# Optimization experiments

Hardware: AMD Instinct MI355X
Metric: run time of the kernel (lower is better)

The kernel has to match this reference:

```python
import jax, jax.numpy as jnp
import numpy as np

N_NODES = 50000
N_EDGES = 800000
D = 128          # input_dim == output_dim
H = 2 * D        # hidden size = 2*output_dim
EPS = 1e-5       # BatchNorm1d eps


def _mlp(x, W1, b1, g1, beta1, W2, b2):
    # Linear -> BatchNorm1d (training-mode batch stats) -> ReLU -> Linear
    y = x @ W1 + b1
    mu = jnp.mean(y, axis=0)
    var = jnp.mean(jnp.square(y - mu), axis=0)  # biased var, as used for normalization
    y = (y - mu) * jax.lax.rsqrt(var + EPS) * g1 + beta1
    y = jax.nn.relu(y)
    return y @ W2 + b2


def setup_inputs() -> dict:
    key = jax.random.key(0)
    ks = jax.random.split(key, 16)
    h = jax.random.normal(ks[0], (N_NODES, D), dtype=jnp.float32)
    e = jax.random.normal(ks[1], (N_EDGES, D), dtype=jnp.float32)
    src = jax.random.randint(ks[2], (N_EDGES,), 0, N_NODES, dtype=jnp.int32)
    dst = jax.random.randint(ks[3], (N_EDGES,), 0, N_NODES, dtype=jnp.int32)

    def lin(k, fan_in, fan_out):
        return jax.random.normal(k, (fan_in, fan_out), dtype=jnp.float32) * (1.0 / np.sqrt(fan_in))

    params = {
        # mlp_bond: in 2D -> H -> D
        'W1b': lin(ks[4], 2 * D, H), 'b1b': jnp.zeros((H,), jnp.float32),
        'g1b': jnp.ones((H,), jnp.float32), 'beta1b': jnp.zeros((H,), jnp.float32),
        'W2b': lin(ks[5], H, D), 'b2b': jnp.zeros((D,), jnp.float32),
        # mlp_atom: in 2D -> H -> D
        'W1a': lin(ks[6], 2 * D, H), 'b1a': jnp.zeros((H,), jnp.float32),
        'g1a': jnp.ones((H,), jnp.float32), 'beta1a': jnp.zeros((H,), jnp.float32),
        'W2a': lin(ks[7], H, D), 'b2a': jnp.zeros((D,), jnp.float32),
    }
    return {'h': h, 'e': e, 'src': src, 'dst': dst, **params}


def reference(h, e, src, dst,
              W1b, b1b, g1b, beta1b, W2b, b2b,
              W1a, b1a, g1a, beta1a, W2a, b2a):
    # --- bond update: gather u_add_v, concat with e, MLP ---
    sum_h_edge = h[src] + h[dst]                              # [E, D]
    e_new = _mlp(jnp.concatenate([sum_h_edge, e], axis=-1),
                 W1b, b1b, g1b, beta1b, W2b, b2b)             # [E, D]

    # --- atom update: scatter-sum of src node feats and NEW edge feats to dst ---
    sum_h = jax.ops.segment_sum(h[src], dst, num_segments=N_NODES)   # copy_u + sum
    sum_e = jax.ops.segment_sum(e_new, dst, num_segments=N_NODES)   # copy_e + sum
    h_new = _mlp(jnp.concatenate([sum_h, sum_e], axis=-1),
                 W1a, b1a, g1a, beta1a, W2a, b2a)             # [N, D]

    # out_batch_norm=False, out_activation=None, residual=False, dropout=None
    return h_new, e_new
```

## Files before the change

kernel.cpp:

```cpp
#include <hip/hip_runtime.h>
#include <stdint.h>

#define DD 128
#define HH 256
#define EPSBN 1e-5f

typedef __attribute__((ext_vector_type(4))) float f32x4;
typedef __attribute__((ext_vector_type(8))) short s16x8;
typedef __attribute__((ext_vector_type(4))) short s16x4;

__device__ __forceinline__ unsigned short f2bf(float f){
  union{float f; unsigned u;} v; v.f=f;
  unsigned u = v.u + 0x7fffu + ((v.u>>16)&1u);
  return (unsigned short)(u>>16);
}
__device__ __forceinline__ float bf2f(unsigned short s){
  union{unsigned u; float f;} v; v.u=((unsigned)s)<<16; return v.f;
}
__device__ __forceinline__ int swz(int row, int kb){ return row*512 + (kb ^ ((row&7)<<4)); }

__global__ void wt_kernel(const float* __restrict__ W1b, const float* __restrict__ W2b,
                          const float* __restrict__ W1a, const float* __restrict__ W2a,
                          unsigned short* __restrict__ WT1b, unsigned short* __restrict__ WT2b,
                          unsigned short* __restrict__ WT1a, unsigned short* __restrict__ WT2a){
  int idx = blockIdx.x*256 + threadIdx.x;
  if (idx < 65536){ int n=idx>>8, k=idx&255; WT1b[n*256+k]=f2bf(W1b[k*256+n]); }
  else if (idx < 98304){ int t=idx-65536; int n=t>>8, k=t&255; WT2b[n*256+k]=f2bf(W2b[k*128+n]); }
  else if (idx < 163840){ int t=idx-98304; int n=t>>8, k=t&255; WT1a[n*256+k]=f2bf(W1a[k*256+n]); }
  else if (idx < 196608){ int t=idx-163840; int n=t>>8, k=t&255; WT2a[n*256+k]=f2bf(W2a[k*128+n]); }
}

__global__ void h2bf_kernel(const float* __restrict__ h, unsigned short* __restrict__ hb, int n8){
  int i = blockIdx.x*256 + threadIdx.x;
  if (i < n8){
    f32x4 a = *(const f32x4*)(h + (size_t)i*8);
    f32x4 b = *(const f32x4*)(h + (size_t)i*8 + 4);
    s16x8 p;
    #pragma unroll
    for (int q=0;q<4;q++){ p[q]=(short)f2bf(a[q]); p[4+q]=(short)f2bf(b[q]); }
    *(s16x8*)(hb + (size_t)i*8) = p;
  }
}

__global__ void hist_kernel(const int* __restrict__ dst, int* __restrict__ counts, int E){
  int i = blockIdx.x*256 + threadIdx.x;
  if (i < E) atomicAdd(&counts[dst[i]], 1);
}

__global__ void scan_kernel(const int* __restrict__ counts, int* __restrict__ offsets,
                            int* __restrict__ cursor, int n){
  __shared__ int wsum[16];
  int tid = threadIdx.x, lane = tid&63, wid = tid>>6;
  int carry = 0;
  int nch = (n + 1023)/1024;
  for (int ch=0; ch<nch; ch++){
    int i = ch*1024 + tid;
    int v = (i<n)? counts[i] : 0;
    int s = v;
    #pragma unroll
    for (int off=1; off<64; off<<=1){ int t = __shfl_up(s, off); if (lane>=off) s += t; }
    if (lane==63) wsum[wid] = s;
    __syncthreads();
    int woff = 0, tot = 0;
    #pragma unroll
    for (int w=0; w<16; w++){ int t = wsum[w]; if (w<wid) woff += t; tot += t; }
    if (i<n){ int excl = carry + woff + s - v; offsets[i]=excl; cursor[i]=excl; }
    carry += tot;
    __syncthreads();
  }
  if (tid==0) offsets[n] = carry;
}

__global__ void fill_kernel(const int* __restrict__ dst, int* __restrict__ cursor,
                            int* __restrict__ eids, int E){
  int i = blockIdx.x*256 + threadIdx.x;
  if (i < E){ int slot = atomicAdd(&cursor[dst[i]], 1); eids[slot] = i; }
}

__device__ __forceinline__ void gemm1_core(char* xt, const s16x8 (&Bf)[8][2],
                                           float bias0, float bias1,
                                           unsigned short* __restrict__ yout,
                                           float* __restrict__ stats,
                                           int base, int nrows)
{
  const int tid = threadIdx.x;
  const int l = tid&63, w = tid>>6, lr = l&15, lg = l>>4;
  const int nb = w*32;
  f32x4 acc[4][2];
  #pragma unroll
  for (int mt=0;mt<4;mt++)
    #pragma unroll
    for (int nt=0;nt<2;nt++) acc[mt][nt] = (f32x4){0.f,0.f,0.f,0.f};
  #pragma unroll
  for (int kc=0;kc<8;kc++){
    s16x8 af[4];
    #pragma unroll
    for (int mt=0;mt<4;mt++)
      af[mt] = *(const s16x8*)(xt + swz(mt*16 + lr, kc*64 + lg*16));
    #pragma unroll
    for (int nt=0;nt<2;nt++)
      #pragma unroll
      for (int mt=0;mt<4;mt++)
        acc[mt][nt] = __builtin_amdgcn_mfma_f32_16x16x32_bf16(af[mt], Bf[kc][nt], acc[mt][nt], 0,0,0);
  }
  float st1a=0.f, st1b=0.f, st2a=0.f, st2b=0.f;
  #pragma unroll
  for (int mt=0;mt<4;mt++)
    #pragma unroll
    for (int q=0;q<4;q++){
      float m = (base + mt*16 + lg*4 + q < nrows) ? 1.0f : 0.0f;
      float v0 = (acc[mt][0][q] + bias0)*m;
      float v1 = (acc[mt][1][q] + bias1)*m;
      st1a += v0; st2a += v0*v0;
      st1b += v1; st2b += v1*v1;
    }
  __syncthreads();
  #pragma unroll
  for (int mt=0;mt<4;mt++)
    #pragma unroll
    for (int q=0;q<4;q++){
      *(unsigned short*)(xt + (mt*16 + lg*4 + q)*512 + (nb + lr)*2)      = f2bf(acc[mt][0][q] + bias0);
      *(unsigned short*)(xt + (mt*16 + lg*4 + q)*512 + (nb + 16 + lr)*2) = f2bf(acc[mt][1][q] + bias1);
    }
  __syncthreads();
  #pragma unroll
  for (int it=0;it<4;it++){
    int off = it*8192 + tid*16;
    int row = off >> 9;
    if (base + row < nrows)
      *(s16x8*)((char*)yout + (size_t)base*512 + off) = *(const s16x8*)(xt + off);
  }
  {
    int rep = blockIdx.x & 63;
    float s;
    s = st1a; s += __shfl_xor(s,16); s += __shfl_xor(s,32);
    if (l < 16) atomicAdd(&stats[rep*512 + nb + lr], s);
    s = st2a; s += __shfl_xor(s,16); s += __shfl_xor(s,32);
    if (l < 16) atomicAdd(&stats[rep*512 + 256 + nb + lr], s);
    s = st1b; s += __shfl_xor(s,16); s += __shfl_xor(s,32);
    if (l < 16) atomicAdd(&stats[rep*512 + nb + 16 + lr], s);
    s = st2b; s += __shfl_xor(s,16); s += __shfl_xor(s,32);
    if (l < 16) atomicAdd(&stats[rep*512 + 256 + nb + 16 + lr], s);
  }
}

__global__ __launch_bounds__(512, 4) void edge_mlp1(
    const unsigned short* __restrict__ hb, const float* __restrict__ e,
    const int* __restrict__ src, const int* __restrict__ dstv,
    const unsigned short* __restrict__ WT1, const float* __restrict__ b1,
    unsigned short* __restrict__ yout, float* __restrict__ stats, int E)
{
  __shared__ alignas(16) char xt[32768];
  const int tid = threadIdx.x;
  const int l = tid&63, w = tid>>6, lr = l&15, lg = l>>4;
  const int nb = w*32;
  const int base = blockIdx.x*64;

  {
    const int cb = tid&31, r0 = tid>>5;
    #pragma unroll
    for (int k=0;k<4;k++){
      int r = r0 + k*16;
      f32x4 v = *(const f32x4*)(e + (size_t)(base+r)*DD + cb*4);
      s16x4 p;
      #pragma unroll
      for (int q=0;q<4;q++) p[q] = (short)f2bf(v[q]);
      *(s16x4*)(xt + swz(r, 256 + cb*8)) = p;
    }
  }
  {
    const int r = tid>>3, jj = tid&7;
    const int ei = base + r;
    int s_ = src[ei], d_ = dstv[ei];
    const s16x8* hs = (const s16x8*)(hb + (size_t)s_*DD) + jj*2;
    const s16x8* hd = (const s16x8*)(hb + (size_t)d_*DD) + jj*2;
    s16x8 a0=hs[0], a1=hs[1], c0=hd[0], c1=hd[1];
    s16x8 o0, o1;
    #pragma unroll
    for (int q=0;q<8;q++){
      o0[q] = (short)f2bf(bf2f((unsigned short)a0[q]) + bf2f((unsigned short)c0[q]));
      o1[q] = (short)f2bf(bf2f((unsigned short)a1[q]) + bf2f((unsigned short)c1[q]));
    }
    *(s16x8*)(xt + swz(r, jj*32))      = o0;
    *(s16x8*)(xt + swz(r, jj*32 + 16)) = o1;
  }
  s16x8 Bf[8][2];
  #pragma unroll
  for (int kc=0;kc<8;kc++)
    #pragma unroll
    for (int nt=0;nt<2;nt++)
      Bf[kc][nt] = *(const s16x8*)(WT1 + (size_t)(nb + nt*16 + lr)*256 + kc*32 + lg*8);
  float bias0 = b1[nb+lr], bias1 = b1[nb+16+lr];
  __syncthreads();
  gemm1_core(xt, Bf, bias0, bias1, yout, stats, base, E);
}

__global__ __launch_bounds__(512, 2) void node_mlp1(
    const unsigned short* __restrict__ hb, const float* __restrict__ enew,
    const int* __restrict__ src, const int* __restrict__ offsets, const int* __restrict__ eids,
    const unsigned short* __restrict__ WT1, const float* __restrict__ b1,
    unsigned short* __restrict__ yout, float* __restrict__ stats, int NN)
{
  __shared__ alignas(16) char xt[32768];
  const int tid = threadIdx.x;
  const int l = tid&63, w = tid>>6, lr = l&15, lg = l>>4;
  const int nb = w*32;
  const int base = blockIdx.x*64;
  const int r = tid>>3, jj = tid&7;
  const int node = base + r;

  float ah[16], ae[16];
  #pragma unroll
  for (int q=0;q<16;q++){ ah[q]=0.f; ae[q]=0.f; }
  if (node < NN){
    int beg = offsets[node], end = offsets[node+1];
    for (int p=beg;p<end;p++){
      int eid = eids[p];
      int s_ = src[eid];
      const s16x8* hs = (const s16x8*)(hb + (size_t)s_*DD + jj*16);
      const f32x4* ep = (const f32x4*)(enew + (size_t)eid*DD + jj*16);
      s16x8 a0 = hs[0], a1 = hs[1];
      f32x4 e0 = ep[0], e1 = ep[1], e2 = ep[2], e3 = ep[3];
      #pragma unroll
      for (int q=0;q<8;q++){ ah[q] += bf2f((unsigned short)a0[q]); ah[8+q] += bf2f((unsigned short)a1[q]); }
      #pragma unroll
      for (int q=0;q<4;q++){ ae[q] += e0[q]; ae[4+q] += e1[q]; ae[8+q] += e2[q]; ae[12+q] += e3[q]; }
    }
  }
  {
    s16x8 o0, o1;
    #pragma unroll
    for (int q=0;q<8;q++){ o0[q] = (short)f2bf(ah[q]); o1[q] = (short)f2bf(ah[8+q]); }
    *(s16x8*)(xt + swz(r, jj*32))      = o0;
    *(s16x8*)(xt + swz(r, jj*32 + 16)) = o1;
    #pragma unroll
    for (int q=0;q<8;q++){ o0[q] = (short)f2bf(ae[q]); o1[q] = (short)f2bf(ae[8+q]); }
    *(s16x8*)(xt + swz(r, 256 + jj*32))      = o0;
    *(s16x8*)(xt + swz(r, 256 + jj*32 + 16)) = o1;
  }
  s16x8 Bf[8][2];
  #pragma unroll
  for (int kc=0;kc<8;kc++)
    #pragma unroll
    for (int nt=0;nt<2;nt++)
      Bf[kc][nt] = *(const s16x8*)(WT1 + (size_t)(nb + nt*16 + lr)*256 + kc*32 + lg*8);
  float bias0 = b1[nb+lr], bias1 = b1[nb+16+lr];
  __syncthreads();
  gemm1_core(xt, Bf, bias0, bias1, yout, stats, base, NN);
}

__global__ void finalize_kernel(const float* __restrict__ stats, const float* __restrict__ g,
                                const float* __restrict__ beta, float* __restrict__ scale, float invcnt){
  __shared__ float red[512];
  int tid = threadIdx.x;
  float s = 0.f;
  for (int rep=0; rep<64; rep++) s += stats[rep*512 + tid];
  red[tid] = s;
  __syncthreads();
  if (tid < 256){
    float mu  = red[tid]*invcnt;
    float var = red[256+tid]*invcnt - mu*mu;
    float a = g[tid] * rsqrtf(var + EPSBN);
    float c = beta[tid] - mu*a;
    scale[2*tid] = a; scale[2*tid+1] = c;
  }
}

__global__ __launch_bounds__(512, 4) void mlp2_kernel(const unsigned short* y,
    const unsigned short* __restrict__ WT2, const float* __restrict__ b2,
    const float* __restrict__ scale, float* outp, int nrows)
{
  __shared__ alignas(16) char xt[32768];
  const int tid = threadIdx.x;
  const int l = tid&63, w = tid>>6, lr = l&15, lg = l>>4;
  const int nb = w*16;
  const int base = blockIdx.x*64;

  const int cb = tid&31, r0 = tid>>5;
  float sa[8], sc[8];
  #pragma unroll
  for (int q=0;q<8;q++){ sa[q]=scale[2*(cb*8+q)]; sc[q]=scale[2*(cb*8+q)+1]; }
  #pragma unroll
  for (int k=0;k<4;k++){
    int r = r0 + k*16;
    s16x8 raw = {0,0,0,0,0,0,0,0};
    if (base + r < nrows) raw = *(const s16x8*)(y + (size_t)(base+r)*HH + cb*8);
    s16x8 o;
    #pragma unroll
    for (int q=0;q<8;q++){
      float f = fmaxf(bf2f((unsigned short)raw[q])*sa[q] + sc[q], 0.0f);
      o[q] = (short)f2bf(f);
    }
    *(s16x8*)(xt + swz(r, cb*16)) = o;
  }
  s16x8 Bf[8];
  #pragma unroll
  for (int kc=0;kc<8;kc++)
    Bf[kc] = *(const s16x8*)(WT2 + (size_t)(nb + lr)*HH + kc*32 + lg*8);
  float bias = b2[nb+lr];
  __syncthreads();

  f32x4 acc[4];
  #pragma unroll
  for (int mt=0;mt<4;mt++) acc[mt] = (f32x4){0.f,0.f,0.f,0.f};
  #pragma unroll
  for (int kc=0;kc<8;kc++){
    s16x8 af[4];
    #pragma unroll
    for (int mt=0;mt<4;mt++)
      af[mt] = *(const s16x8*)(xt + swz(mt*16 + lr, kc*64 + lg*16));
    #pragma unroll
    for (int mt=0;mt<4;mt++)
      acc[mt] = __builtin_amdgcn_mfma_f32_16x16x32_bf16(af[mt], Bf[kc], acc[mt], 0,0,0);
  }
  __syncthreads();
  #pragma unroll
  for (int mt=0;mt<4;mt++)
    #pragma unroll
    for (int q=0;q<4;q++)
      *(float*)(xt + (mt*16 + lg*4 + q)*512 + (nb + lr)*4) = acc[mt][q] + bias;
  __syncthreads();
  #pragma unroll
  for (int it=0;it<4;it++){
    int off = it*8192 + tid*16;
    int row = off >> 9;
    if (base + row < nrows)
      *(f32x4*)(outp + (size_t)(base+row)*DD + ((off&511)>>2)) = *(const f32x4*)(xt + off);
  }
}

extern "C" void kernel_launch(void* const* d_in, const int* in_sizes, int n_in,
                              void* d_out, int out_size, void* d_ws, size_t ws_size,
                              hipStream_t stream) {
  const float* h    = (const float*)d_in[0];
  const float* e    = (const float*)d_in[1];
  const int*   src  = (const int*)d_in[2];
  const int*   dst  = (const int*)d_in[3];
  const float* W1b  = (const float*)d_in[4];
  const float* b1b  = (const float*)d_in[5];
  const float* g1b  = (const float*)d_in[6];
  const float* beta1b=(const float*)d_in[7];
  const float* W2b  = (const float*)d_in[8];
  const float* b2b  = (const float*)d_in[9];
  const float* W1a  = (const float*)d_in[10];
  const float* b1a  = (const float*)d_in[11];
  const float* g1a  = (const float*)d_in[12];
  const float* beta1a=(const float*)d_in[13];
  const float* W2a  = (const float*)d_in[14];
  const float* b2a  = (const float*)d_in[15];

  const int E  = in_sizes[2];
  const int NN = in_sizes[0] / DD;

  char* ws = (char*)d_ws;
  unsigned short* WT1b = (unsigned short*)(ws + 0);
  unsigned short* WT2b = (unsigned short*)(ws + 131072);
  unsigned short* WT1a = (unsigned short*)(ws + 196608);
  unsigned short* WT2a = (unsigned short*)(ws + 327680);
  float* scaleE = (float*)(ws + 393216);
  float* scaleN = (float*)(ws + 395264);
  float* statsE = (float*)(ws + 397312);
  float* statsN = (float*)(ws + 528384);
  int* counts  = (int*)(ws + 659456);
  int* offsets = (int*)(ws + 860160);
  int* cursor  = (int*)(ws + 1060864);
  int* eids    = (int*)(ws + 1261568);
  unsigned short* ya = (unsigned short*)(ws + 4461568);
  unsigned short* hb = (unsigned short*)(ws + 30086144);

  float* outH = (float*)d_out;
  float* outE = outH + (size_t)NN * DD;
  unsigned short* yE = (unsigned short*)outE;

  hipMemsetAsync(ws + 397312, 0, 131072 + 131072 + 200704, stream);

  wt_kernel<<<768, 256, 0, stream>>>(W1b, W2b, W1a, W2a, WT1b, WT2b, WT1a, WT2a);
  h2bf_kernel<<<(NN*DD/8 + 255)/256, 256, 0, stream>>>(h, hb, NN*DD/8);
  hist_kernel<<<(E+255)/256, 256, 0, stream>>>(dst, counts, E);
  scan_kernel<<<1, 1024, 0, stream>>>(counts, offsets, cursor, NN);
  fill_kernel<<<(E+255)/256, 256, 0, stream>>>(dst, cursor, eids, E);

  const int tE = E/64;
  const int tN = (NN + 63)/64;

  edge_mlp1<<<tE, 512, 0, stream>>>(hb, e, src, dst, WT1b, b1b, yE, statsE, E);
  finalize_kernel<<<1, 512, 0, stream>>>(statsE, g1b, beta1b, scaleE, 1.0f/(float)E);
  mlp2_kernel<<<tE, 512, 0, stream>>>(yE, WT2b, b2b, scaleE, outE, E);
  node_mlp1<<<tN, 512, 0, stream>>>(hb, outE, src, offsets, eids, WT1a, b1a, ya, statsN, NN);
  finalize_kernel<<<1, 512, 0, stream>>>(statsN, g1a, beta1a, scaleN, 1.0f/(float)NN);
  mlp2_kernel<<<tN, 512, 0, stream>>>(ya, WT2a, b2a, scaleN, outH, NN);
}
```

Before: 800.5 us.

## Split node gather from GEMM, process two tiles per block, widen swizzle

The node MLP's first stage is split in two. A separate high-occupancy gather kernel accumulates the per-node h and e sums into a bf16 buffer, which reuses the output region as scratch, and a plain GEMM kernel then reads that buffer. Before, the gather ran inside a 2-waves-per-SIMD GEMM kernel. Edge MLP1 and MLP2 now process two 64-row tiles per block, so the weight fragments are loaded once per block and amortised over more rows. The swizzle XOR is widened from 3 to 5 row bits, and f2bf now calls the HIP intrinsic. These changes add an extra global round-trip for the node inputs, and the new swizzle could change LDS bank behaviour in either direction.

```diff
diff --git a/kernel.cpp b/kernel.cpp
--- a/kernel.cpp
+++ b/kernel.cpp
@@ -1,4 +1,5 @@
 #include <hip/hip_runtime.h>
+#include <hip/hip_bf16.h>
 #include <stdint.h>
 
 #define DD 128
@@ -10,14 +11,14 @@
 typedef __attribute__((ext_vector_type(4))) short s16x4;
 
 __device__ __forceinline__ unsigned short f2bf(float f){
-  union{float f; unsigned u;} v; v.f=f;
-  unsigned u = v.u + 0x7fffu + ((v.u>>16)&1u);
-  return (unsigned short)(u>>16);
+  union { __hip_bfloat16 h; unsigned short u; } v;
+  v.h = __float2bfloat16(f);
+  return v.u;
 }
 __device__ __forceinline__ float bf2f(unsigned short s){
   union{unsigned u; float f;} v; v.u=((unsigned)s)<<16; return v.f;
 }
-__device__ __forceinline__ int swz(int row, int kb){ return row*512 + (kb ^ ((row&7)<<4)); }
+__device__ __forceinline__ int swz(int row, int kb){ return row*512 + (kb ^ ((row&31)<<4)); }
 
 __global__ void wt_kernel(const float* __restrict__ W1b, const float* __restrict__ W2b,
                           const float* __restrict__ W1a, const float* __restrict__ W2a,
@@ -77,58 +78,109 @@
   if (i < E){ int slot = atomicAdd(&cursor[dst[i]], 1); eids[slot] = i; }
 }
 
-__device__ __forceinline__ void gemm1_core(char* xt, const s16x8 (&Bf)[8][2],
-                                           float bias0, float bias1,
-                                           unsigned short* __restrict__ yout,
-                                           float* __restrict__ stats,
-                                           int base, int nrows)
-{
+__device__ __forceinline__ void stage_edge_tile(char* xt,
+    const unsigned short* __restrict__ hb, const float* __restrict__ e,
+    const int* __restrict__ src, const int* __restrict__ dstv, int base)
+{
+  const int tid = threadIdx.x;
+  {
+    const int cb = tid&31, r0 = tid>>5;
+    #pragma unroll
+    for (int k=0;k<4;k++){
+      int r = r0 + k*16;
+      f32x4 v = *(const f32x4*)(e + (size_t)(base+r)*DD + cb*4);
+      s16x4 p;
+      #pragma unroll
+      for (int q=0;q<4;q++) p[q] = (short)f2bf(v[q]);
+      *(s16x4*)(xt + swz(r, 256 + cb*8)) = p;
+    }
+  }
+  {
+    const int r = tid>>3, jj = tid&7;
+    const int ei = base + r;
+    int s_ = src[ei], d_ = dstv[ei];
+    const s16x8* hs = (const s16x8*)(hb + (size_t)s_*DD) + jj*2;
+    const s16x8* hd = (const s16x8*)(hb + (size_t)d_*DD) + jj*2;
+    s16x8 a0=hs[0], a1=hs[1], c0=hd[0], c1=hd[1];
+    s16x8 o0, o1;
+    #pragma unroll
+    for (int q=0;q<8;q++){
+      o0[q] = (short)f2bf(bf2f((unsigned short)a0[q]) + bf2f((unsigned short)c0[q]));
+      o1[q] = (short)f2bf(bf2f((unsigned short)a1[q]) + bf2f((unsigned short)c1[q]));
+    }
+    *(s16x8*)(xt + swz(r, jj*32))      = o0;
+    *(s16x8*)(xt + swz(r, jj*32 + 16)) = o1;
+  }
+}
+
+__global__ __launch_bounds__(512, 4) void edge_mlp1(
+    const unsigned short* __restrict__ hb, const float* __restrict__ e,
+    const int* __restrict__ src, const int* __restrict__ dstv,
+    const unsigned short* __restrict__ WT1, const float* __restrict__ b1,
+    unsigned short* __restrict__ yout, float* __restrict__ stats, int E)
+{
+  __shared__ alignas(16) char xt[32768];
   const int tid = threadIdx.x;
   const int l = tid&63, w = tid>>6, lr = l&15, lg = l>>4;
   const int nb = w*32;
-  f32x4 acc[4][2];
-  #pragma unroll
-  for (int mt=0;mt<4;mt++)
-    #pragma unroll
-    for (int nt=0;nt<2;nt++) acc[mt][nt] = (f32x4){0.f,0.f,0.f,0.f};
-  #pragma unroll
-  for (int kc=0;kc<8;kc++){
-    s16x8 af[4];
+  const int base0 = blockIdx.x*128;
+
+  s16x8 Bf[8][2];
+  #pragma unroll
+  for (int kc=0;kc<8;kc++)
+    #pragma unroll
+    for (int nt=0;nt<2;nt++)
+      Bf[kc][nt] = *(const s16x8*)(WT1 + (size_t)(nb + nt*16 + lr)*256 + kc*32 + lg*8);
+  float bias0 = b1[nb+lr], bias1 = b1[nb+16+lr];
+
+  float st1a=0.f, st1b=0.f, st2a=0.f, st2b=0.f;
+
+  #pragma unroll 1
+  for (int t=0;t<2;t++){
+    const int base = base0 + t*64;
+    stage_edge_tile(xt, hb, e, src, dstv, base);
+    __syncthreads();
+    f32x4 acc[4][2];
     #pragma unroll
     for (int mt=0;mt<4;mt++)
-      af[mt] = *(const s16x8*)(xt + swz(mt*16 + lr, kc*64 + lg*16));
-    #pragma unroll
-    for (int nt=0;nt<2;nt++)
+      #pragma unroll
+      for (int nt=0;nt<2;nt++) acc[mt][nt] = (f32x4){0.f,0.f,0.f,0.f};
+    #pragma unroll
+    for (int kc=0;kc<8;kc++){
+      s16x8 af[4];
       #pragma unroll
       for (int mt=0;mt<4;mt++)
-        acc[mt][nt] = __builtin_amdgcn_mfma_f32_16x16x32_bf16(af[mt], Bf[kc][nt], acc[mt][nt], 0,0,0);
-  }
-  float st1a=0.f, st1b=0.f, st2a=0.f, st2b=0.f;
-  #pragma unroll
-  for (int mt=0;mt<4;mt++)
-    #pragma unroll
-    for (int q=0;q<4;q++){
-      float m = (base + mt*16 + lg*4 + q < nrows) ? 1.0f : 0.0f;
-      float v0 = (acc[mt][0][q] + bias0)*m;
-      float v1 = (acc[mt][1][q] + bias1)*m;
-      st1a += v0; st2a += v0*v0;
-      st1b += v1; st2b += v1*v1;
-    }
-  __syncthreads();
-  #pragma unroll
-  for (int mt=0;mt<4;mt++)
-    #pragma unroll
-    for (int q=0;q<4;q++){
-      *(unsigned short*)(xt + (mt*16 + lg*4 + q)*512 + (nb + lr)*2)      = f2bf(acc[mt][0][q] + bias0);
-      *(unsigned short*)(xt + (mt*16 + lg*4 + q)*512 + (nb + 16 + lr)*2) = f2bf(acc[mt][1][q] + bias1);
-    }
-  __syncthreads();
-  #pragma unroll
-  for (int it=0;it<4;it++){
-    int off = it*8192 + tid*16;
-    int row = off >> 9;
-    if (base + row < nrows)
+        af[mt] = *(const s16x8*)(xt + swz(mt*16 + lr, kc*64 + lg*16));
+      #pragma unroll
+      for (int nt=0;nt<2;nt++)
+        #pragma unroll
+        for (int mt=0;mt<4;mt++)
+          acc[mt][nt] = __builtin_amdgcn_mfma_f32_16x16x32_bf16(af[mt], Bf[kc][nt], acc[mt][nt], 0,0,0);
+    }
+    #pragma unroll
+    for (int mt=0;mt<4;mt++)
+      #pragma unroll
+      for (int q=0;q<4;q++){
+        float v0 = acc[mt][0][q] + bias0;
+        float v1 = acc[mt][1][q] + bias1;
+        st1a += v0; st2a += v0*v0;
+        st1b += v1; st2b += v1*v1;
+      }
+    __syncthreads();
+    #pragma unroll
+    for (int mt=0;mt<4;mt++)
+      #pragma unroll
+      for (int q=0;q<4;q++){
+        *(unsigned short*)(xt + (mt*16 + lg*4 + q)*512 + (nb + lr)*2)      = f2bf(acc[mt][0][q] + bias0);
+        *(unsigned short*)(xt + (mt*16 + lg*4 + q)*512 + (nb + 16 + lr)*2) = f2bf(acc[mt][1][q] + bias1);
+      }
+    __syncthreads();
+    #pragma unroll
+    for (int it=0;it<4;it++){
+      int off = it*8192 + tid*16;
       *(s16x8*)((char*)yout + (size_t)base*512 + off) = *(const s16x8*)(xt + off);
+    }
+    if (t==0) __syncthreads();
   }
   {
     int rep = blockIdx.x & 63;
@@ -144,11 +196,181 @@
   }
 }
 
-__global__ __launch_bounds__(512, 4) void edge_mlp1(
-    const unsigned short* __restrict__ hb, const float* __restrict__ e,
-    const int* __restrict__ src, const int* __restrict__ dstv,
+__global__ __launch_bounds__(512, 4) void mlp2_kernel(const unsigned short* y,
+    const unsigned short* __restrict__ WT2, const float* __restrict__ b2,
+    const float* __restrict__ scale, float* outp, int nrows)
+{
+  __shared__ alignas(16) char xt[32768];
+  const int tid = threadIdx.x;
+  const int l = tid&63, w = tid>>6, lr = l&15, lg = l>>4;
+  const int nb = w*16;
+  const int base0 = blockIdx.x*128;
+
+  s16x8 Bf[8];
+  #pragma unroll
+  for (int kc=0;kc<8;kc++)
+    Bf[kc] = *(const s16x8*)(WT2 + (size_t)(nb + lr)*HH + kc*32 + lg*8);
+  float bias = b2[nb+lr];
+  const int cb = tid&31, r0 = tid>>5;
+  float sa[8], sc[8];
+  #pragma unroll
+  for (int q=0;q<8;q++){ sa[q]=scale[2*(cb*8+q)]; sc[q]=scale[2*(cb*8+q)+1]; }
+
+  #pragma unroll 1
+  for (int t=0;t<2;t++){
+    const int base = base0 + t*64;
+    #pragma unroll
+    for (int k=0;k<4;k++){
+      int r = r0 + k*16;
+      s16x8 raw = {0,0,0,0,0,0,0,0};
+      if (base + r < nrows) raw = *(const s16x8*)(y + (size_t)(base+r)*HH + cb*8);
+      s16x8 o;
+      #pragma unroll
+      for (int q=0;q<8;q++){
+        float f = fmaxf(bf2f((unsigned short)raw[q])*sa[q] + sc[q], 0.0f);
+        o[q] = (short)f2bf(f);
+      }
+      *(s16x8*)(xt + swz(r, cb*16)) = o;
+    }
+    __syncthreads();
+    f32x4 acc[4];
+    #pragma unroll
+    for (int mt=0;mt<4;mt++) acc[mt] = (f32x4){0.f,0.f,0.f,0.f};
+    #pragma unroll
+    for (int kc=0;kc<8;kc++){
+      s16x8 af[4];
+      #pragma unroll
+      for (int mt=0;mt<4;mt++)
+        af[mt] = *(const s16x8*)(xt + swz(mt*16 + lr, kc*64 + lg*16));
+      #pragma unroll
+      for (int mt=0;mt<4;mt++)
+        acc[mt] = __builtin_amdgcn_mfma_f32_16x16x32_bf16(af[mt], Bf[kc], acc[mt], 0,0,0);
+    }
+    __syncthreads();
+    #pragma unroll
+    for (int mt=0;mt<4;mt++)
+      #pragma unroll
+      for (int q=0;q<4;q++)
+        *(float*)(xt + (mt*16 + lg*4 + q)*512 + (nb + lr)*4) = acc[mt][q] + bias;
+    __syncthreads();
+    #pragma unroll
+    for (int it=0;it<4;it++){
+      int off = it*8192 + tid*16;
+      int row = off >> 9;
+      if (base + row < nrows)
+        *(f32x4*)(outp + (size_t)(base+row)*DD + ((off&511)>>2)) = *(const f32x4*)(xt + off);
+    }
+    if (t==0) __syncthreads();
+  }
+}
+
+__global__ __launch_bounds__(256, 8) void node_gather(
+    const unsigned short* __restrict__ hb, const float* __restrict__ enew,
+    const int* __restrict__ src, const int* __restrict__ offsets, const int* __restrict__ eids,
+    unsigned short* __restrict__ xnode, int NN)
+{
+  const int tid = threadIdx.x;
+  const int r = tid>>3, jj = tid&7;
+  const int node = blockIdx.x*32 + r;
+  if (node >= NN) return;
+  float ah[16], ae[16];
+  #pragma unroll
+  for (int q=0;q<16;q++){ ah[q]=0.f; ae[q]=0.f; }
+  int beg = offsets[node], end = offsets[node+1];
+  for (int p=beg;p<end;p++){
+    int eid = eids[p];
+    int s_ = src[eid];
+    const s16x8* hs = (const s16x8*)(hb + (size_t)s_*DD + jj*16);
+    const f32x4* ep = (const f32x4*)(enew + (size_t)eid*DD + jj*16);
+    s16x8 a0 = hs[0], a1 = hs[1];
+    f32x4 e0 = ep[0], e1 = ep[1], e2 = ep[2], e3 = ep[3];
+    #pragma unroll
+    for (int q=0;q<8;q++){ ah[q] += bf2f((unsigned short)a0[q]); ah[8+q] += bf2f((unsigned short)a1[q]); }
+    #pragma unroll
+    for (int q=0;q<4;q++){ ae[q] += e0[q]; ae[4+q] += e1[q]; ae[8+q] += e2[q]; ae[12+q] += e3[q]; }
+  }
+  s16x8 o0, o1;
+  #pragma unroll
+  for (int q=0;q<8;q++){ o0[q] = (short)f2bf(ah[q]); o1[q] = (short)f2bf(ah[8+q]); }
+  *(s16x8*)(xnode + (size_t)node*HH + jj*16)     = o0;
+  *(s16x8*)(xnode + (size_t)node*HH + jj*16 + 8) = o1;
+  #pragma unroll
+  for (int q=0;q<8;q++){ o0[q] = (short)f2bf(ae[q]); o1[q] = (short)f2bf(ae[8+q]); }
+  *(s16x8*)(xnode + (size_t)node*HH + 128 + jj*16)     = o0;
+  *(s16x8*)(xnode + (size_t)node*HH + 128 + jj*16 + 8) = o1;
+}
+
+__device__ __forceinline__ void gemm1_core(char* xt, const s16x8 (&Bf)[8][2],
+                                           float bias0, float bias1,
+                                           unsigned short* __restrict__ yout,
+                                           float* __restrict__ stats,
+                                           int base, int nrows)
+{
+  const int tid = threadIdx.x;
+  const int l = tid&63, w = tid>>6, lr = l&15, lg = l>>4;
+  const int nb = w*32;
+  f32x4 acc[4][2];
+  #pragma unroll
+  for (int mt=0;mt<4;mt++)
+    #pragma unroll
+    for (int nt=0;nt<2;nt++) acc[mt][nt] = (f32x4){0.f,0.f,0.f,0.f};
+  #pragma unroll
+  for (int kc=0;kc<8;kc++){
+    s16x8 af[4];
+    #pragma unroll
+    for (int mt=0;mt<4;mt++)
+      af[mt] = *(const s16x8*)(xt + swz(mt*16 + lr, kc*64 + lg*16));
+    #pragma unroll
+    for (int nt=0;nt<2;nt++)
+      #pragma unroll
+      for (int mt=0;mt<4;mt++)
+        acc[mt][nt] = __builtin_amdgcn_mfma_f32_16x16x32_bf16(af[mt], Bf[kc][nt], acc[mt][nt], 0,0,0);
+  }
+  float st1a=0.f, st1b=0.f, st2a=0.f, st2b=0.f;
+  #pragma unroll
+  for (int mt=0;mt<4;mt++)
+    #pragma unroll
+    for (int q=0;q<4;q++){
+      float m = (base + mt*16 + lg*4 + q < nrows) ? 1.0f : 0.0f;
+      float v0 = (acc[mt][0][q] + bias0)*m;
+      float v1 = (acc[mt][1][q] + bias1)*m;
+      st1a += v0; st2a += v0*v0;
+      st1b += v1; st2b += v1*v1;
+    }
+  __syncthreads();
+  #pragma unroll
+  for (int mt=0;mt<4;mt++)
+    #pragma unroll
+    for (int q=0;q<4;q++){
+      *(unsigned short*)(xt + (mt*16 + lg*4 + q)*512 + (nb + lr)*2)      = f2bf(acc[mt][0][q] + bias0);
+      *(unsigned short*)(xt + (mt*16 + lg*4 + q)*512 + (nb + 16 + lr)*2) = f2bf(acc[mt][1][q] + bias1);
+    }
+  __syncthreads();
+  #pragma unroll
+  for (int it=0;it<4;it++){
+    int off = it*8192 + tid*16;
+    int row = off >> 9;
+    if (base + row < nrows)
+      *(s16x8*)((char*)yout + (size_t)base*512 + off) = *(const s16x8*)(xt + off);
+  }
+  {
+    int rep = blockIdx.x & 63;
+    float s;
+    s = st1a; s += __shfl_xor(s,16); s += __shfl_xor(s,32);
+    if (l < 16) atomicAdd(&stats[rep*512 + nb + lr], s);
+    s = st2a; s += __shfl_xor(s,16); s += __shfl_xor(s,32);
+    if (l < 16) atomicAdd(&stats[rep*512 + 256 + nb + lr], s);
+    s = st1b; s += __shfl_xor(s,16); s += __shfl_xor(s,32);
+    if (l < 16) atomicAdd(&stats[rep*512 + nb + 16 + lr], s);
+    s = st2b; s += __shfl_xor(s,16); s += __shfl_xor(s,32);
+    if (l < 16) atomicAdd(&stats[rep*512 + 256 + nb + 16 + lr], s);
+  }
+}
+
+__global__ __launch_bounds__(512, 4) void node_gemm1(
+    const unsigned short* __restrict__ xnode,
     const unsigned short* __restrict__ WT1, const float* __restrict__ b1,
-    unsigned short* __restrict__ yout, float* __restrict__ stats, int E)
+    unsigned short* __restrict__ yout, float* __restrict__ stats, int NN)
 {
   __shared__ alignas(16) char xt[32768];
   const int tid = threadIdx.x;
@@ -156,87 +378,13 @@
   const int nb = w*32;
   const int base = blockIdx.x*64;
 
-  {
-    const int cb = tid&31, r0 = tid>>5;
-    #pragma unroll
-    for (int k=0;k<4;k++){
-      int r = r0 + k*16;
-      f32x4 v = *(const f32x4*)(e + (size_t)(base+r)*DD + cb*4);
-      s16x4 p;
-      #pragma unroll
-      for (int q=0;q<4;q++) p[q] = (short)f2bf(v[q]);
-      *(s16x4*)(xt + swz(r, 256 + cb*8)) = p;
-    }
-  }
-  {
-    const int r = tid>>3, jj = tid&7;
-    const int ei = base + r;
-    int s_ = src[ei], d_ = dstv[ei];
-    const s16x8* hs = (const s16x8*)(hb + (size_t)s_*DD) + jj*2;
-    const s16x8* hd = (const s16x8*)(hb + (size_t)d_*DD) + jj*2;
-    s16x8 a0=hs[0], a1=hs[1], c0=hd[0], c1=hd[1];
-    s16x8 o0, o1;
-    #pragma unroll
-    for (int q=0;q<8;q++){
-      o0[q] = (short)f2bf(bf2f((unsigned short)a0[q]) + bf2f((unsigned short)c0[q]));
-      o1[q] = (short)f2bf(bf2f((unsigned short)a1[q]) + bf2f((unsigned short)c1[q]));
-    }
-    *(s16x8*)(xt + swz(r, jj*32))      = o0;
-    *(s16x8*)(xt + swz(r, jj*32 + 16)) = o1;
-  }
-  s16x8 Bf[8][2];
-  #pragma unroll
-  for (int kc=0;kc<8;kc++)
-    #pragma unroll
-    for (int nt=0;nt<2;nt++)
-      Bf[kc][nt] = *(const s16x8*)(WT1 + (size_t)(nb + nt*16 + lr)*256 + kc*32 + lg*8);
-  float bias0 = b1[nb+lr], bias1 = b1[nb+16+lr];
-  __syncthreads();
-  gemm1_core(xt, Bf, bias0, bias1, yout, stats, base, E);
-}
-
-__global__ __launch_bounds__(512, 2) void node_mlp1(
-    const unsigned short* __restrict__ hb, const float* __restrict__ enew,
-    const int* __restrict__ src, const int* __restrict__ offsets, const int* __restrict__ eids,
-    const unsigned short* __restrict__ WT1, const float* __restrict__ b1,
-    unsigned short* __restrict__ yout, float* __restrict__ stats, int NN)
-{
-  __shared__ alignas(16) char xt[32768];
-  const int tid = threadIdx.x;
-  const int l = tid&63, w = tid>>6, lr = l&15, lg = l>>4;
-  const int nb = w*32;
-  const int base = blockIdx.x*64;
-  const int r = tid>>3, jj = tid&7;
-  const int node = base + r;
-
-  float ah[16], ae[16];
-  #pragma unroll
-  for (int q=0;q<16;q++){ ah[q]=0.f; ae[q]=0.f; }
-  if (node < NN){
-    int beg = offsets[node], end = offsets[node+1];
-    for (int p=beg;p<end;p++){
-      int eid = eids[p];
-      int s_ = src[eid];
-      const s16x8* hs = (const s16x8*)(hb + (size_t)s_*DD + jj*16);
-      const f32x4* ep = (const f32x4*)(enew + (size_t)eid*DD + jj*16);
-      s16x8 a0 = hs[0], a1 = hs[1];
-      f32x4 e0 = ep[0], e1 = ep[1], e2 = ep[2], e3 = ep[3];
-      #pragma unroll
-      for (int q=0;q<8;q++){ ah[q] += bf2f((unsigned short)a0[q]); ah[8+q] += bf2f((unsigned short)a1[q]); }
-      #pragma unroll
-      for (int q=0;q<4;q++){ ae[q] += e0[q]; ae[4+q] += e1[q]; ae[8+q] += e2[q]; ae[12+q] += e3[q]; }
-    }
-  }
-  {
-    s16x8 o0, o1;
-    #pragma unroll
-    for (int q=0;q<8;q++){ o0[q] = (short)f2bf(ah[q]); o1[q] = (short)f2bf(ah[8+q]); }
-    *(s16x8*)(xt + swz(r, jj*32))      = o0;
-    *(s16x8*)(xt + swz(r, jj*32 + 16)) = o1;
-    #pragma unroll
-    for (int q=0;q<8;q++){ o0[q] = (short)f2bf(ae[q]); o1[q] = (short)f2bf(ae[8+q]); }
-    *(s16x8*)(xt + swz(r, 256 + jj*32))      = o0;
-    *(s16x8*)(xt + swz(r, 256 + jj*32 + 16)) = o1;
+  #pragma unroll
+  for (int it=0;it<4;it++){
+    int off = it*8192 + tid*16;
+    int row = off >> 9, kb = off & 511;
+    s16x8 v = {0,0,0,0,0,0,0,0};
+    if (base + row < NN) v = *(const s16x8*)((const char*)xnode + (size_t)base*512 + off);
+    *(s16x8*)(xt + swz(row, kb)) = v;
   }
   s16x8 Bf[8][2];
   #pragma unroll
@@ -263,69 +411,6 @@
     float a = g[tid] * rsqrtf(var + EPSBN);
     float c = beta[tid] - mu*a;
     scale[2*tid] = a; scale[2*tid+1] = c;
-  }
-}
-
-__global__ __launch_bounds__(512, 4) void mlp2_kernel(const unsigned short* y,
-    const unsigned short* __restrict__ WT2, const float* __restrict__ b2,
-    const float* __restrict__ scale, float* outp, int nrows)
-{
-  __shared__ alignas(16) char xt[32768];
-  const int tid = threadIdx.x;
-  const int l = tid&63, w = tid>>6, lr = l&15, lg = l>>4;
-  const int nb = w*16;
-  const int base = blockIdx.x*64;
-
-  const int cb = tid&31, r0 = tid>>5;
-  float sa[8], sc[8];
-  #pragma unroll
-  for (int q=0;q<8;q++){ sa[q]=scale[2*(cb*8+q)]; sc[q]=scale[2*(cb*8+q)+1]; }
-  #pragma unroll
-  for (int k=0;k<4;k++){
-    int r = r0 + k*16;
-    s16x8 raw = {0,0,0,0,0,0,0,0};
-    if (base + r < nrows) raw = *(const s16x8*)(y + (size_t)(base+r)*HH + cb*8);
-    s16x8 o;
-    #pragma unroll
-    for (int q=0;q<8;q++){
-      float f = fmaxf(bf2f((unsigned short)raw[q])*sa[q] + sc[q], 0.0f);
-      o[q] = (short)f2bf(f);
-    }
-    *(s16x8*)(xt + swz(r, cb*16)) = o;
-  }
-  s16x8 Bf[8];
-  #pragma unroll
-  for (int kc=0;kc<8;kc++)
-    Bf[kc] = *(const s16x8*)(WT2 + (size_t)(nb + lr)*HH + kc*32 + lg*8);
-  float bias = b2[nb+lr];
-  __syncthreads();
-
-  f32x4 acc[4];
-  #pragma unroll
-  for (int mt=0;mt<4;mt++) acc[mt] = (f32x4){0.f,0.f,0.f,0.f};
-  #pragma unroll
-  for (int kc=0;kc<8;kc++){
-    s16x8 af[4];
-    #pragma unroll
-    for (int mt=0;mt<4;mt++)
-      af[mt] = *(const s16x8*)(xt + swz(mt*16 + lr, kc*64 + lg*16));
-    #pragma unroll
-    for (int mt=0;mt<4;mt++)
-      acc[mt] = __builtin_amdgcn_mfma_f32_16x16x32_bf16(af[mt], Bf[kc], acc[mt], 0,0,0);
-  }
-  __syncthreads();
-  #pragma unroll
-  for (int mt=0;mt<4;mt++)
-    #pragma unroll
-    for (int q=0;q<4;q++)
-      *(float*)(xt + (mt*16 + lg*4 + q)*512 + (nb + lr)*4) = acc[mt][q] + bias;
-  __syncthreads();
-  #pragma unroll
-  for (int it=0;it<4;it++){
-    int off = it*8192 + tid*16;
-    int row = off >> 9;
-    if (base + row < nrows)
-      *(f32x4*)(outp + (size_t)(base+row)*DD + ((off&511)>>2)) = *(const f32x4*)(xt + off);
   }
 }
 
@@ -371,6 +456,7 @@
   float* outH = (float*)d_out;
   float* outE = outH + (size_t)NN * DD;
   unsigned short* yE = (unsigned short*)outE;
+  unsigned short* xnode = (unsigned short*)outH;
 
   hipMemsetAsync(ws + 397312, 0, 131072 + 131072 + 200704, stream);
 
@@ -380,13 +466,16 @@
   scan_kernel<<<1, 1024, 0, stream>>>(counts, offsets, cursor, NN);
   fill_kernel<<<(E+255)/256, 256, 0, stream>>>(dst, cursor, eids, E);
 
-  const int tE = E/64;
-  const int tN = (NN + 63)/64;
-
-  edge_mlp1<<<tE, 512, 0, stream>>>(hb, e, src, dst, WT1b, b1b, yE, statsE, E);
+  const int tE128 = E/128;
+  const int tN64  = (NN + 63)/64;
+  const int tN128 = (NN + 127)/128;
+  const int gG    = (NN + 31)/32;
+
+  edge_mlp1<<<tE128, 512, 0, stream>>>(hb, e, src, dst, WT1b, b1b, yE, statsE, E);
   finalize_kernel<<<1, 512, 0, stream>>>(statsE, g1b, beta1b, scaleE, 1.0f/(float)E);
-  mlp2_kernel<<<tE, 512, 0, stream>>>(yE, WT2b, b2b, scaleE, outE, E);
-  node_mlp1<<<tN, 512, 0, stream>>>(hb, outE, src, offsets, eids, WT1a, b1a, ya, statsN, NN);
+  mlp2_kernel<<<tE128, 512, 0, stream>>>(yE, WT2b, b2b, scaleE, outE, E);
+  node_gather<<<gG, 256, 0, stream>>>(hb, outE, src, offsets, eids, xnode, NN);
+  node_gemm1<<<tN64, 512, 0, stream>>>(xnode, WT1a, b1a, ya, statsN, NN);
   finalize_kernel<<<1, 512, 0, stream>>>(statsN, g1a, beta1a, scaleN, 1.0f/(float)NN);
-  mlp2_kernel<<<tN, 512, 0, stream>>>(ya, WT2a, b2a, scaleN, outH, NN);
-}
+  mlp2_kernel<<<tN128, 512, 0, stream>>>(ya, WT2a, b2a, scaleN, outH, NN);
+}
```

New measurement: 1.291 ms. +61.3%, slower.
